# Kernel tuning notes

Hardware: AMD Instinct MI355X
Metric: run time of the kernel (lower is better)

Reference implementation:

```python
import jax, jax.numpy as jnp
import numpy as np

NUM_CLASSES = 100
CACHE_SIZE = 50
N_PROTOS = NUM_CLASSES * CACHE_SIZE  # 5000
FEAT_DIM = 128
BATCH = 2048
NVIEWS = 2
TEMP = 0.1
EPSILON = 0.05
PROTO_M = 0.99
TOPK = 10
LAMBDA_PCON = 1.0
SINKHORN_ITERS = 3


def _l1norm(x, axis):
    return x / jnp.clip(jnp.sum(jnp.abs(x), axis=axis, keepdims=True), 1e-12)


def _l2norm(x, axis=-1):
    return x / jnp.clip(jnp.linalg.norm(x, axis=axis, keepdims=True), 1e-12)


def _sinkhorn(feats, protos):
    # torch uses out.detach(): Q carries no gradient
    out = jax.lax.stop_gradient(feats @ protos.T)  # [N, K]
    Q = jnp.exp(out / EPSILON).T                   # [K, N]
    K_, B_ = Q.shape
    Q = Q / jnp.sum(Q)
    for _ in range(SINKHORN_ITERS):
        Q = _l1norm(Q, axis=1) / K_   # row L1 normalize
        Q = _l1norm(Q, axis=0) / B_   # col L1 normalize
    return (Q * B_).T                 # [N, K]


def _topk_mask(x, k):
    _, idx = jax.lax.top_k(x, k)
    rows = jnp.arange(x.shape[0])[:, None]
    return jnp.zeros_like(x).at[rows, idx].set(1.0)


def reference(features, targets, beta, protos):
    # features: [B, V, D] -> [V*B, D] (view-major, matches torch.cat(torch.unbind(dim=1)))
    feats = jnp.transpose(features, (1, 0, 2)).reshape(-1, FEAT_DIM)
    labels = jnp.tile(targets, NVIEWS)                              # [N]
    contrast_labels = jnp.tile(jnp.arange(NUM_CLASSES), CACHE_SIZE)  # [K]
    mask = (labels[:, None] == contrast_labels[None, :]).astype(feats.dtype)  # [N, K]

    # ---- mle_loss ----
    Q = _sinkhorn(feats, jax.lax.stop_gradient(protos))
    update_mask = mask * Q
    tkm = _topk_mask(update_mask, TOPK)
    update_mask = _l1norm(tkm * update_mask, axis=1)

    update_features = update_mask.T @ feats                         # [K, D]
    protos_new = PROTO_M * protos + (1.0 - PROTO_M) * update_features
    sim_mean = jax.lax.stop_gradient(
        jnp.mean(jnp.sum(_l2norm(update_features, 1) * _l2norm(protos, 1), axis=1)))
    protos2 = _l2norm(protos_new, axis=1)

    Q2 = _sinkhorn(feats, jax.lax.stop_gradient(protos2))
    logits = jax.nn.softplus(feats @ jax.lax.stop_gradient(protos2).T / TEMP)  # [N, K]

    loss_mask = mask * Q2
    # NOTE: original code top-ks update_mask (already normalized) here, not loss_mask
    tkm2 = _topk_mask(update_mask, TOPK)
    loss_mask = _l1norm(tkm2 * loss_mask, axis=1)
    masked_logits = loss_mask * logits

    positive_logits = mask * logits
    negative_logits = logits * (1.0 - mask)
    imp = jax.lax.stop_gradient(jnp.exp(beta * jnp.log(negative_logits + 1e-10)))
    total_logits = positive_logits + imp * negative_logits

    pos = jnp.sum(masked_logits, axis=1)                             # [N]
    neg = jnp.log(jnp.sum(jnp.exp(total_logits), axis=1, keepdims=True))  # [N, 1]
    # faithful to the torch broadcast: [N] - [N,1] -> [N, N]
    mle = -jnp.mean(pos - neg)

    # ---- proto_contra ----
    pn = _l2norm(protos2, axis=1)                                    # [K, D]
    plabels = jnp.tile(jnp.arange(NUM_CLASSES), CACHE_SIZE)
    pmask = (plabels[:, None] == plabels[None, :]).astype(pn.dtype)
    tau = jax.lax.stop_gradient((1.0 + (0.5 - sim_mean)) * 0.4)
    adc = pn @ pn.T / tau
    lg = adc - jax.lax.stop_gradient(jnp.max(adc, axis=1, keepdims=True))
    lmask = 1.0 - jnp.eye(N_PROTOS, dtype=pn.dtype)
    pmask = pmask * lmask
    ppos = jnp.sum(_l1norm(pmask, axis=1) * lg, axis=1)
    pneg = jnp.log(jnp.sum(lmask * jnp.exp(lg), axis=1))
    pcon = -jnp.mean(ppos - pneg)

    return mle + LAMBDA_PCON * pcon


def setup_inputs() -> dict:
    key = jax.random.key(0)
    k1, k2, k3 = jax.random.split(key, 3)
    features = jax.random.normal(k1, (BATCH, NVIEWS, FEAT_DIM), dtype=jnp.float32)
    features = _l2norm(features, axis=-1)  # unit-norm embeddings keep exp(./eps) finite
    targets = jax.random.randint(k2, (BATCH,), 0, NUM_CLASSES)
    beta = jnp.float32(0.5)
    protos = _l2norm(jax.random.uniform(k3, (N_PROTOS, FEAT_DIM), dtype=jnp.float32), axis=-1)
    return {"features": features, "targets": targets, "beta": beta, "protos": protos}
```

## Files before the change

kernel.cpp:

```cpp
#include <hip/hip_runtime.h>
#include <math.h>

constexpr int NUM_CLASSES = 100;
constexpr int CACHE_SIZE  = 50;
constexpr int NPROT       = 5000;
constexpr int FD          = 128;
constexpr int BATCH       = 2048;
constexpr int NROWS       = 4096;
constexpr int TOPK        = 10;
constexpr float INV_EPS   = 20.0f;
constexpr float INV_TEMP  = 10.0f;
constexpr float PROTO_M   = 0.99f;
constexpr int PLD         = 5120;
constexpr int SROWS       = 16;
constexpr int NSLOT       = NROWS / SROWS;
constexpr int NTILE       = 40;
constexpr int NTRI        = NTILE * (NTILE + 1) / 2;

typedef __attribute__((ext_vector_type(8))) short bf16x8;
typedef __attribute__((ext_vector_type(4))) float f32x4;
typedef __attribute__((ext_vector_type(4))) _Float16 f16x4;
typedef __attribute__((ext_vector_type(8))) _Float16 f16x8;

__device__ __forceinline__ float blockReduceSum(float v) {
  __shared__ float tmp[8];
  const int lane = threadIdx.x & 63;
  const int wid  = threadIdx.x >> 6;
  #pragma unroll
  for (int o = 32; o > 0; o >>= 1) v += __shfl_down(v, o, 64);
  __syncthreads();
  if (lane == 0) tmp[wid] = v;
  __syncthreads();
  const int nw = (blockDim.x + 63) >> 6;
  float s = 0.f;
  for (int i = 0; i < nw; ++i) s += tmp[i];
  return s;
}

__device__ __forceinline__ short f2bf(float x) {
  union { float f; unsigned u; } v; v.f = x;
  const unsigned r = v.u + 0x7fffu + ((v.u >> 16) & 1u);
  return (short)(r >> 16);
}
__device__ __forceinline__ float bf2f(short h) {
  union { float f; unsigned u; } v; v.u = ((unsigned)(unsigned short)h) << 16;
  return v.f;
}

__device__ __forceinline__ float fast_softplus(float x) {
  return fmaxf(x, 0.f) + __logf(1.f + __expf(-fabsf(x)));
}

__global__ void k_build_split(const float* __restrict__ features,
                              const float* __restrict__ protos,
                              float* __restrict__ feats,
                              short* __restrict__ fhi, short* __restrict__ flo,
                              short* __restrict__ phi, short* __restrict__ plo) {
  constexpr int NF4 = NROWS * (FD / 4);
  constexpr int NP4 = NPROT * FD / 4;
  const int t = blockIdx.x * 256 + threadIdx.x;
  if (t < NF4) {
    const int n  = t >> 5;
    const int d4 = (t & 31) << 2;
    const int b  = n & (BATCH - 1);
    const int v  = n >> 11;
    const float4 src = *reinterpret_cast<const float4*>(features + ((size_t)b * 2 + v) * FD + d4);
    *reinterpret_cast<float4*>(feats + (size_t)n * FD + d4) = src;
    short4 h, l;
    h.x = f2bf(src.x); l.x = f2bf(src.x - bf2f(h.x));
    h.y = f2bf(src.y); l.y = f2bf(src.y - bf2f(h.y));
    h.z = f2bf(src.z); l.z = f2bf(src.z - bf2f(h.z));
    h.w = f2bf(src.w); l.w = f2bf(src.w - bf2f(h.w));
    *reinterpret_cast<short4*>(fhi + (size_t)n * FD + d4) = h;
    *reinterpret_cast<short4*>(flo + (size_t)n * FD + d4) = l;
  } else if (t - NF4 < NP4) {
    const int u = t - NF4;
    const float4 v = *reinterpret_cast<const float4*>(protos + (size_t)u * 4);
    short4 h, l;
    h.x = f2bf(v.x); l.x = f2bf(v.x - bf2f(h.x));
    h.y = f2bf(v.y); l.y = f2bf(v.y - bf2f(h.y));
    h.z = f2bf(v.z); l.z = f2bf(v.z - bf2f(h.z));
    h.w = f2bf(v.w); l.w = f2bf(v.w - bf2f(h.w));
    *reinterpret_cast<short4*>(phi + (size_t)u * 4) = h;
    *reinterpret_cast<short4*>(plo + (size_t)u * 4) = l;
  }
}

__global__ __launch_bounds__(256) void k_gemm_mfma(
    const short* __restrict__ Ahi, const short* __restrict__ Alo,
    const short* __restrict__ Bhi, const short* __restrict__ Blo,
    int Nb, _Float16* __restrict__ C, float* __restrict__ colpart) {
  __shared__ __align__(16) short Bs[2][128 * 64];
  __shared__ float red[4][128];
  const int tid  = threadIdx.x;
  const int wid  = tid >> 6;
  const int lane = tid & 63;
  const int lr   = lane & 15;
  const int kg   = lane >> 4;
  const int m0   = blockIdx.y * 128 + wid * 32;
  const int n0   = blockIdx.x * 128;

  f32x4 acc[2][8];
  #pragma unroll
  for (int i = 0; i < 2; ++i)
    #pragma unroll
    for (int j = 0; j < 8; ++j) acc[i][j] = (f32x4){0.f, 0.f, 0.f, 0.f};

  bool cval[8];
  #pragma unroll
  for (int j = 0; j < 8; ++j) cval[j] = (n0 + j * 16 + lr < Nb);

  const int scol = tid >> 1;
  const int sk   = (tid & 1) * 32;
  const int gcol = min(n0 + scol, Nb - 1);

  #pragma unroll
  for (int h = 0; h < 2; ++h) {
    const int k0 = h * 64;
    if (h) __syncthreads();
    #pragma unroll
    for (int u = 0; u < 4; ++u) {
      const int kk2 = sk + u * 8;
      const bf16x8 vh = *reinterpret_cast<const bf16x8*>(Bhi + (size_t)gcol * FD + k0 + kk2);
      const bf16x8 vl = *reinterpret_cast<const bf16x8*>(Blo + (size_t)gcol * FD + k0 + kk2);
      const int byteoff = (scol * 128 + kk2 * 2) ^ ((scol & 7) << 4);
      *reinterpret_cast<bf16x8*>(reinterpret_cast<char*>(&Bs[0][0]) + byteoff) = vh;
      *reinterpret_cast<bf16x8*>(reinterpret_cast<char*>(&Bs[1][0]) + byteoff) = vl;
    }
    __syncthreads();
    #pragma unroll
    for (int kk = 0; kk < 2; ++kk) {
      const int kb = k0 + kk * 32 + kg * 8;
      bf16x8 ah[2], al[2], bh[8], bl[8];
      #pragma unroll
      for (int i = 0; i < 2; ++i) {
        const size_t off = (size_t)(m0 + i * 16 + lr) * FD + kb;
        ah[i] = *reinterpret_cast<const bf16x8*>(Ahi + off);
        al[i] = *reinterpret_cast<const bf16x8*>(Alo + off);
      }
      #pragma unroll
      for (int j = 0; j < 8; ++j) {
        const int col = j * 16 + lr;
        const int bo = (col * 128 + (kk * 32 + kg * 8) * 2) ^ ((col & 7) << 4);
        bh[j] = *reinterpret_cast<const bf16x8*>(reinterpret_cast<const char*>(&Bs[0][0]) + bo);
        bl[j] = *reinterpret_cast<const bf16x8*>(reinterpret_cast<const char*>(&Bs[1][0]) + bo);
      }
      #pragma unroll
      for (int i = 0; i < 2; ++i)
        #pragma unroll
        for (int j = 0; j < 8; ++j) {
          acc[i][j] = __builtin_amdgcn_mfma_f32_16x16x32_bf16(ah[i], bh[j], acc[i][j], 0, 0, 0);
          acc[i][j] = __builtin_amdgcn_mfma_f32_16x16x32_bf16(ah[i], bl[j], acc[i][j], 0, 0, 0);
          acc[i][j] = __builtin_amdgcn_mfma_f32_16x16x32_bf16(al[i], bh[j], acc[i][j], 0, 0, 0);
        }
    }
  }

  float csum[8];
  #pragma unroll
  for (int j = 0; j < 8; ++j) csum[j] = 0.f;
  #pragma unroll
  for (int i = 0; i < 2; ++i) {
    const int rbase = m0 + i * 16 + kg * 4;
    #pragma unroll
    for (int j = 0; j < 8; ++j) {
      if (!cval[j]) continue;
      const int col = n0 + j * 16 + lr;
      #pragma unroll
      for (int q = 0; q < 4; ++q) {
        const _Float16 hv = (_Float16)acc[i][j][q];
        C[(size_t)(rbase + q) * NPROT + col] = hv;
        csum[j] += __expf((float)hv * INV_EPS);
      }
    }
  }
  __syncthreads();
  #pragma unroll
  for (int j = 0; j < 8; ++j) {
    float v = csum[j];
    v += __shfl_xor(v, 16, 64);
    v += __shfl_xor(v, 32, 64);
    if (lane < 16) red[wid][j * 16 + lane] = v;
  }
  __syncthreads();
  if (tid < 128) {
    const int col = n0 + tid;
    if (col < Nb) {
      const float t = red[0][tid] + red[1][tid] + red[2][tid] + red[3][tid];
      colpart[(size_t)blockIdx.y * PLD + col] = t;
    }
  }
}

template <bool WITH_MLE>
__global__ __launch_bounds__(512) void k_sink_fused(const _Float16* __restrict__ big,
                                                    const float* __restrict__ Rin,
                                                    float* __restrict__ part,
                                                    float* __restrict__ semain,
                                                    const float* __restrict__ beta_ptr) {
  __shared__ float Cl[SROWS];
  const int r0   = blockIdx.x * SROWS;
  const int wid  = threadIdx.x >> 6;
  const int lane = threadIdx.x & 63;
  float beta = 0.f;
  bool bhalf = false;
  if constexpr (WITH_MLE) {
    beta = beta_ptr[0];
    bhalf = (beta == 0.5f);
  }
  #pragma unroll
  for (int rr = 0; rr < SROWS / 8; ++rr) {
    const int r = rr * 8 + wid;
    const _Float16* row = big + (size_t)(r0 + r) * NPROT;
    float s = 0.f, se = 0.f;
    for (int idx = lane; idx < NPROT / 8; idx += 64) {
      const f16x8 v = *reinterpret_cast<const f16x8*>(row + idx * 8);
      const float4 q0 = *reinterpret_cast<const float4*>(Rin + idx * 8);
      const float4 q1 = *reinterpret_cast<const float4*>(Rin + idx * 8 + 4);
      float ro[8];
      #pragma unroll
      for (int e = 0; e < 8; ++e) ro[e] = (float)v[e];
      s = fmaf(__expf(ro[0] * INV_EPS), q0.x, s);
      s = fmaf(__expf(ro[1] * INV_EPS), q0.y, s);
      s = fmaf(__expf(ro[2] * INV_EPS), q0.z, s);
      s = fmaf(__expf(ro[3] * INV_EPS), q0.w, s);
      s = fmaf(__expf(ro[4] * INV_EPS), q1.x, s);
      s = fmaf(__expf(ro[5] * INV_EPS), q1.y, s);
      s = fmaf(__expf(ro[6] * INV_EPS), q1.z, s);
      s = fmaf(__expf(ro[7] * INV_EPS), q1.w, s);
      if constexpr (WITH_MLE) {
        #pragma unroll
        for (int e = 0; e < 8; ++e) {
          const float x = ro[e] * INV_TEMP;
          const float l = fast_softplus(x);
          const float lb = l + 1e-10f;
          const float imp = bhalf ? sqrtf(lb) : __expf(beta * __logf(lb));
          se += __expf(imp * l);
        }
      }
    }
    #pragma unroll
    for (int o = 32; o > 0; o >>= 1) {
      s += __shfl_down(s, o, 64);
      if constexpr (WITH_MLE) se += __shfl_down(se, o, 64);
    }
    if (lane == 0) {
      Cl[r] = 1.0f / s;
      if constexpr (WITH_MLE) semain[r0 + r] = se;
    }
  }
  __syncthreads();
  for (int k4 = threadIdx.x * 4; k4 < NPROT; k4 += 2048) {
    float s[4] = {0.f, 0.f, 0.f, 0.f};
    #pragma unroll
    for (int r = 0; r < SROWS; ++r) {
      const f16x4 v = *reinterpret_cast<const f16x4*>(big + (size_t)(r0 + r) * NPROT + k4);
      const float c = Cl[r];
      #pragma unroll
      for (int e = 0; e < 4; ++e) s[e] = fmaf(__expf((float)v[e] * INV_EPS), c, s[e]);
    }
    *reinterpret_cast<float4*>(part + (size_t)blockIdx.x * PLD + k4) =
        make_float4(s[0], s[1], s[2], s[3]);
  }
}

__global__ __launch_bounds__(512) void k_red_slots(const float* __restrict__ part,
                                                   int nslots, float* __restrict__ R) {
  __shared__ float red[8][64];
  const int g  = threadIdx.x >> 6;
  const int kk = threadIdx.x & 63;
  const int k  = blockIdx.x * 64 + kk;
  float s = 0.f;
  if (k < NPROT) {
    const int per = nslots >> 3;
    const int b0 = g * per, b1 = b0 + per;
    for (int b = b0; b < b1; ++b) s += part[(size_t)b * PLD + k];
  }
  red[g][kk] = s;
  __syncthreads();
  if (threadIdx.x < 64 && k < NPROT) {
    float t = 0.f;
    #pragma unroll
    for (int g2 = 0; g2 < 8; ++g2) t += red[g2][kk];
    R[k] = 1.0f / t;
  }
}

__global__ __launch_bounds__(256) void k_top10(const _Float16* __restrict__ out1,
                                               const float* __restrict__ R3,
                                               const int* __restrict__ targets,
                                               float* __restrict__ wsel) {
  const int n = blockIdx.x * 4 + (threadIdx.x >> 6);
  const int lane = threadIdx.x & 63;
  const int c = targets[n & (BATCH - 1)];
  float cur = -1.0f, orig = -1.0f;
  if (lane < CACHE_SIZE) {
    const int k = c + lane * NUM_CLASSES;
    cur = __expf((float)out1[(size_t)n * NPROT + k] * INV_EPS) * R3[k];
    orig = cur;
  }
  float tvsum = 0.f;
  bool selme = false;
  #pragma unroll
  for (int i = 0; i < TOPK; ++i) {
    float bv = cur;
    int   bj = lane;
    #pragma unroll
    for (int o = 32; o > 0; o >>= 1) {
      const float ov = __shfl_xor(bv, o, 64);
      const int   oj = __shfl_xor(bj, o, 64);
      if (ov > bv || (ov == bv && oj < bj)) { bv = ov; bj = oj; }
    }
    tvsum += bv;
    if (lane == bj) { cur = -2.0f; selme = true; }
  }
  tvsum = fmaxf(tvsum, 1e-12f);
  if (lane < CACHE_SIZE)
    wsel[(size_t)n * CACHE_SIZE + lane] = selme ? orig / tvsum : 0.f;
}

__global__ __launch_bounds__(1024) void k_prep(const int* __restrict__ targets,
                                               int* __restrict__ classbase,
                                               int* __restrict__ rowlist) {
  __shared__ int t[BATCH];
  __shared__ short chcnt[8][NUM_CLASSES];
  __shared__ int   chpre[8][NUM_CLASSES];
  __shared__ int   ctot[NUM_CLASSES];
  __shared__ int   base[NUM_CLASSES + 1];
  for (int i = threadIdx.x; i < BATCH; i += 1024) t[i] = targets[i];
  __syncthreads();
  if (threadIdx.x < 8 * NUM_CLASSES) {
    const int ch = threadIdx.x / NUM_CLASSES;
    const int c  = threadIdx.x % NUM_CLASSES;
    int m = 0;
    const int i0 = ch << 8;
    for (int i = i0; i < i0 + 256; ++i) m += (t[i] == c);
    chcnt[ch][c] = (short)m;
  }
  __syncthreads();
  if (threadIdx.x < NUM_CLASSES) {
    const int c = threadIdx.x;
    int s = 0;
    #pragma unroll
    for (int ch = 0; ch < 8; ++ch) { chpre[ch][c] = s; s += chcnt[ch][c]; }
    ctot[c] = s;
  }
  __syncthreads();
  if (threadIdx.x == 0) {
    int s = 0;
    for (int c = 0; c < NUM_CLASSES; ++c) { base[c] = s; s += 2 * ctot[c]; }
    base[NUM_CLASSES] = s;
  }
  __syncthreads();
  if (threadIdx.x <= NUM_CLASSES) classbase[threadIdx.x] = base[threadIdx.x];
  for (int b = threadIdx.x; b < BATCH; b += 1024) {
    const int c  = t[b];
    const int ch = b >> 8;
    int r = chpre[ch][c];
    for (int i = ch << 8; i < b; ++i) r += (t[i] == c);
    const int bs  = base[c];
    const int cnt = (base[c + 1] - bs) >> 1;
    rowlist[bs + r] = b;
    rowlist[bs + cnt + r] = BATCH + b;
  }
}

__global__ __launch_bounds__(128) void k_ufpu(const float* __restrict__ feats,
                                              const float* __restrict__ wsel,
                                              const int* __restrict__ rowlist,
                                              const int* __restrict__ classbase,
                                              const float* __restrict__ protos,
                                              short* __restrict__ pnhi,
                                              short* __restrict__ pnlo,
                                              float* __restrict__ simbuf) {
  const int k = blockIdx.x;
  const int d = threadIdx.x;
  const int c = k % NUM_CLASSES;
  const int j = k / NUM_CLASSES;
  const int b0 = classbase[c], b1 = classbase[c + 1];
  float u = 0.f;
  for (int ii = b0; ii < b1; ++ii) {
    const int n = rowlist[ii];
    const float wv = wsel[(size_t)n * CACHE_SIZE + j];
    if (wv != 0.f) u = fmaf(wv, feats[(size_t)n * FD + d], u);
  }
  const float p = protos[(size_t)k * FD + d];
  const float pnew = PROTO_M * p + (1.0f - PROTO_M) * u;
  const float spp = blockReduceSum(p * p);
  const float suu = blockReduceSum(u * u);
  const float sup = blockReduceSum(u * p);
  const float snn = blockReduceSum(pnew * pnew);
  const float x = pnew / fmaxf(sqrtf(snn), 1e-12f);
  const short h = f2bf(x);
  pnhi[(size_t)k * FD + d] = h;
  pnlo[(size_t)k * FD + d] = f2bf(x - bf2f(h));
  if (d == 0)
    simbuf[k] = sup / (fmaxf(sqrtf(suu), 1e-12f) * fmaxf(sqrtf(spp), 1e-12f));
}

__global__ void k_tau(const float* __restrict__ simbuf, float* __restrict__ scalars) {
  float s = 0.f;
  for (int k = threadIdx.x; k < NPROT; k += 256) s += simbuf[k];
  s = blockReduceSum(s);
  if (threadIdx.x == 0) {
    const float sim_mean = s / (float)NPROT;
    scalars[0] = (1.0f + (0.5f - sim_mean)) * 0.4f;
  }
}

__global__ __launch_bounds__(256) void k_mle_fin(const _Float16* __restrict__ out2,
                                                 const float* __restrict__ R3,
                                                 const int* __restrict__ targets,
                                                 const float* __restrict__ wsel,
                                                 const float* __restrict__ beta_ptr,
                                                 const float* __restrict__ semain,
                                                 float* __restrict__ rowres) {
  const int n = blockIdx.x * 4 + (threadIdx.x >> 6);
  const int lane = threadIdx.x & 63;
  const int c = targets[n & (BATCH - 1)];
  const float beta = beta_ptr[0];
  const bool bhalf = (beta == 0.5f);
  float corr = 0.f, swl = 0.f, sw = 0.f;
  if (lane < CACHE_SIZE) {
    const int k = c + lane * NUM_CLASSES;
    const float o = (float)out2[(size_t)n * NPROT + k];
    const float x = o * INV_TEMP;
    const float l = fast_softplus(x);
    const float lb = l + 1e-10f;
    const float imp = bhalf ? sqrtf(lb) : __expf(beta * __logf(lb));
    corr = __expf(l) - __expf(imp * l);
    if (wsel[(size_t)n * CACHE_SIZE + lane] > 0.f) {
      const float w2 = __expf(o * INV_EPS) * R3[k];
      swl = w2 * l;
      sw  = w2;
    }
  }
  #pragma unroll
  for (int o = 32; o > 0; o >>= 1) {
    corr += __shfl_down(corr, o, 64);
    swl  += __shfl_down(swl,  o, 64);
    sw   += __shfl_down(sw,   o, 64);
  }
  if (lane == 0)
    rowres[n] = __logf(semain[n] + corr) - swl / fmaxf(sw, 1e-12f);
}

__global__ __launch_bounds__(256) void k_pcon_mfma(
    const short* __restrict__ Phi, const short* __restrict__ Plo,
    const float* __restrict__ scalars,
    float* __restrict__ part_neg, float* __restrict__ part_pos) {
  __shared__ __align__(16) short Bs[2][128 * 64];
  int tdec = blockIdx.x, by = 0;
  while (tdec >= NTILE - by) { tdec -= NTILE - by; ++by; }
  const int bx = by + tdec;
  const bool diag = (bx == by);

  const int tid  = threadIdx.x;
  const int wid  = tid >> 6;
  const int lane = tid & 63;
  const int lr   = lane & 15;
  const int kg   = lane >> 4;
  const int k0r  = by * 128 + wid * 32;
  const int l0   = bx * 128;
  const float invtau = 1.0f / scalars[0];

  f32x4 acc[2][8];
  #pragma unroll
  for (int i = 0; i < 2; ++i)
    #pragma unroll
    for (int j = 0; j < 8; ++j) acc[i][j] = (f32x4){0.f, 0.f, 0.f, 0.f};

  int rowa[2];
  #pragma unroll
  for (int i = 0; i < 2; ++i) {
    const int r = k0r + i * 16 + lr;
    rowa[i] = (r < NPROT) ? r : (NPROT - 1);
  }
  bool cval[8];
  #pragma unroll
  for (int j = 0; j < 8; ++j) cval[j] = (l0 + j * 16 + lr < NPROT);

  const int scol = tid >> 1;
  const int sk   = (tid & 1) * 32;
  const int gcol = min(l0 + scol, NPROT - 1);

  #pragma unroll
  for (int h = 0; h < 2; ++h) {
    const int k0 = h * 64;
    if (h) __syncthreads();
    #pragma unroll
    for (int u = 0; u < 4; ++u) {
      const int kk2 = sk + u * 8;
      const bf16x8 vh = *reinterpret_cast<const bf16x8*>(Phi + (size_t)gcol * FD + k0 + kk2);
      const bf16x8 vl = *reinterpret_cast<const bf16x8*>(Plo + (size_t)gcol * FD + k0 + kk2);
      const int byteoff = (scol * 128 + kk2 * 2) ^ ((scol & 7) << 4);
      *reinterpret_cast<bf16x8*>(reinterpret_cast<char*>(&Bs[0][0]) + byteoff) = vh;
      *reinterpret_cast<bf16x8*>(reinterpret_cast<char*>(&Bs[1][0]) + byteoff) = vl;
    }
    __syncthreads();
    #pragma unroll
    for (int kk = 0; kk < 2; ++kk) {
      const int kb = k0 + kk * 32 + kg * 8;
      bf16x8 ah[2], al[2], bh[8], bl[8];
      #pragma unroll
      for (int i = 0; i < 2; ++i) {
        const size_t off = (size_t)rowa[i] * FD + kb;
        ah[i] = *reinterpret_cast<const bf16x8*>(Phi + off);
        al[i] = *reinterpret_cast<const bf16x8*>(Plo + off);
      }
      #pragma unroll
      for (int j = 0; j < 8; ++j) {
        const int col = j * 16 + lr;
        const int bo = (col * 128 + (kk * 32 + kg * 8) * 2) ^ ((col & 7) << 4);
        bh[j] = *reinterpret_cast<const bf16x8*>(reinterpret_cast<const char*>(&Bs[0][0]) + bo);
        bl[j] = *reinterpret_cast<const bf16x8*>(reinterpret_cast<const char*>(&Bs[1][0]) + bo);
      }
      #pragma unroll
      for (int i = 0; i < 2; ++i)
        #pragma unroll
        for (int j = 0; j < 8; ++j) {
          acc[i][j] = __builtin_amdgcn_mfma_f32_16x16x32_bf16(ah[i], bh[j], acc[i][j], 0, 0, 0);
          acc[i][j] = __builtin_amdgcn_mfma_f32_16x16x32_bf16(ah[i], bl[j], acc[i][j], 0, 0, 0);
          acc[i][j] = __builtin_amdgcn_mfma_f32_16x16x32_bf16(al[i], bh[j], acc[i][j], 0, 0, 0);
        }
    }
  }

  int ccls[8];
  #pragma unroll
  for (int j = 0; j < 8; ++j) ccls[j] = (l0 + j * 16 + lr) % NUM_CLASSES;
  float cneg[8], cpos[8];
  #pragma unroll
  for (int j = 0; j < 8; ++j) { cneg[j] = 0.f; cpos[j] = 0.f; }

  #pragma unroll
  for (int i = 0; i < 2; ++i) {
    float sneg[4] = {0.f, 0.f, 0.f, 0.f};
    float spos[4] = {0.f, 0.f, 0.f, 0.f};
    const int rbase = k0r + i * 16 + kg * 4;
    #pragma unroll
    for (int q = 0; q < 4; ++q) {
      const int rg = rbase + q;
      if (rg >= NPROT) continue;
      const int rcls = rg % NUM_CLASSES;
      #pragma unroll
      for (int j = 0; j < 8; ++j) {
        const int cg = l0 + j * 16 + lr;
        if (!cval[j]) continue;
        if (diag && cg == rg) continue;
        const float lg = fmaf(acc[i][j][q], invtau, -invtau);
        const float e  = __expf(lg);
        sneg[q] += e;
        cneg[j] += e;
        if (ccls[j] == rcls) { spos[q] += lg; cpos[j] += lg; }
      }
    }
    #pragma unroll
    for (int q = 0; q < 4; ++q) {
      float sn = sneg[q], sp = spos[q];
      #pragma unroll
      for (int off = 8; off > 0; off >>= 1) {
        sn += __shfl_xor(sn, off, 64);
        sp += __shfl_xor(sp, off, 64);
      }
      if (lr == 0) {
        const int rg = rbase + q;
        if (rg < NPROT) {
          part_neg[(size_t)bx * PLD + rg] = sn;
          part_pos[(size_t)bx * PLD + rg] = sp;
        }
      }
    }
  }

  if (!diag) {
    __syncthreads();
    float* redn = reinterpret_cast<float*>(&Bs[0][0]);
    float* redp = redn + 512;
    #pragma unroll
    for (int j = 0; j < 8; ++j) {
      float cn = cneg[j];
      cn += __shfl_xor(cn, 16, 64);
      cn += __shfl_xor(cn, 32, 64);
      float cp = cpos[j];
      cp += __shfl_xor(cp, 16, 64);
      cp += __shfl_xor(cp, 32, 64);
      if (lane < 16) {
        redn[wid * 128 + j * 16 + lane] = cn;
        redp[wid * 128 + j * 16 + lane] = cp;
      }
    }
    __syncthreads();
    if (tid < 128) {
      const int cg = l0 + tid;
      if (cg < NPROT) {
        const float tn = redn[tid] + redn[128 + tid] + redn[256 + tid] + redn[384 + tid];
        const float tp = redp[tid] + redp[128 + tid] + redp[256 + tid] + redp[384 + tid];
        part_neg[(size_t)by * PLD + cg] = tn;
        part_pos[(size_t)by * PLD + cg] = tp;
      }
    }
  }
}

__global__ __launch_bounds__(256) void k_pcon_fin(const float* __restrict__ part_neg,
                                                  const float* __restrict__ part_pos,
                                                  float* __restrict__ pconbuf) {
  __shared__ float rn[4][64], rp[4][64];
  const int g  = threadIdx.x >> 6;
  const int kk = threadIdx.x & 63;
  const int k  = blockIdx.x * 64 + kk;
  float sn = 0.f, sp = 0.f;
  if (k < NPROT) {
    for (int b = g * 10; b < g * 10 + 10; ++b) {
      sn += part_neg[(size_t)b * PLD + k];
      sp += part_pos[(size_t)b * PLD + k];
    }
  }
  rn[g][kk] = sn; rp[g][kk] = sp;
  __syncthreads();
  if (threadIdx.x < 64 && k < NPROT) {
    const float tn = rn[0][kk] + rn[1][kk] + rn[2][kk] + rn[3][kk];
    const float tp = rp[0][kk] + rp[1][kk] + rp[2][kk] + rp[3][kk];
    pconbuf[k] = __logf(tn) - tp * (1.0f / (float)(CACHE_SIZE - 1));
  }
}

__global__ void k_final(const float* __restrict__ rowres,
                        const float* __restrict__ pconbuf,
                        float* __restrict__ outp) {
  float s1 = 0.f, s2 = 0.f;
  for (int i = threadIdx.x; i < NROWS; i += 256) s1 += rowres[i];
  for (int i = threadIdx.x; i < NPROT; i += 256) s2 += pconbuf[i];
  s1 = blockReduceSum(s1);
  s2 = blockReduceSum(s2);
  if (threadIdx.x == 0) outp[0] = s1 / (float)NROWS + s2 / (float)NPROT;
}

extern "C" void kernel_launch(void* const* d_in, const int* in_sizes, int n_in,
                              void* d_out, int out_size, void* d_ws, size_t ws_size,
                              hipStream_t stream) {
  (void)in_sizes; (void)n_in; (void)out_size; (void)ws_size;
  const float* features = (const float*)d_in[0];
  const int*   targets  = (const int*)d_in[1];
  const float* beta     = (const float*)d_in[2];
  const float* protos   = (const float*)d_in[3];
  float* outp = (float*)d_out;

  char* basep = (char*)d_ws;
  size_t off = 0;
  auto alloc = [&](size_t bytes) -> void* {
    void* p = basep + off;
    off = (off + bytes + 255) & ~(size_t)255;
    return p;
  };
  _Float16* big  = (_Float16*)alloc((size_t)NROWS * NPROT * 2);
  float* feats   = (float*)alloc((size_t)NROWS * FD * 4);
  short* fhi     = (short*)alloc((size_t)NROWS * FD * 2);
  short* flo     = (short*)alloc((size_t)NROWS * FD * 2);
  short* phi     = (short*)alloc((size_t)NPROT * FD * 2);
  short* plo     = (short*)alloc((size_t)NPROT * FD * 2);
  float* part    = (float*)alloc((size_t)NSLOT * PLD * 4);
  float* Rk      = (float*)alloc(NPROT * 4);
  float* wsel    = (float*)alloc((size_t)NROWS * CACHE_SIZE * 4);
  int*   rowlist = (int*)alloc(NROWS * 4);
  int*   classbase = (int*)alloc((NUM_CLASSES + 1) * 4);
  float* simbuf  = (float*)alloc(NPROT * 4);
  float* scalars = (float*)alloc(64);
  float* semain  = (float*)alloc(NROWS * 4);
  float* rowres  = (float*)alloc(NROWS * 4);
  float* pconbuf = (float*)alloc(NPROT * 4);
  float* pneg    = (float*)alloc((size_t)NTILE * PLD * 4);
  float* ppos    = (float*)alloc((size_t)NTILE * PLD * 4);

  k_build_split<<<1138, 256, 0, stream>>>(features, protos, feats, fhi, flo, phi, plo);
  k_prep<<<1, 1024, 0, stream>>>(targets, classbase, rowlist);

  k_gemm_mfma<<<dim3(40, 32), 256, 0, stream>>>(fhi, flo, phi, plo, NPROT, big, part);
  k_red_slots<<<79, 512, 0, stream>>>(part, 32, Rk);
  k_sink_fused<false><<<NSLOT, 512, 0, stream>>>(big, Rk, part, nullptr, nullptr);
  k_red_slots<<<79, 512, 0, stream>>>(part, NSLOT, Rk);
  k_sink_fused<false><<<NSLOT, 512, 0, stream>>>(big, Rk, part, nullptr, nullptr);
  k_red_slots<<<79, 512, 0, stream>>>(part, NSLOT, Rk);

  k_top10<<<NROWS / 4, 256, 0, stream>>>(big, Rk, targets, wsel);
  k_ufpu<<<NPROT, 128, 0, stream>>>(feats, wsel, rowlist, classbase, protos, phi, plo, simbuf);
  k_tau<<<1, 256, 0, stream>>>(simbuf, scalars);

  k_gemm_mfma<<<dim3(40, 32), 256, 0, stream>>>(fhi, flo, phi, plo, NPROT, big, part);
  k_red_slots<<<79, 512, 0, stream>>>(part, 32, Rk);
  k_sink_fused<false><<<NSLOT, 512, 0, stream>>>(big, Rk, part, nullptr, nullptr);
  k_red_slots<<<79, 512, 0, stream>>>(part, NSLOT, Rk);
  k_sink_fused<true><<<NSLOT, 512, 0, stream>>>(big, Rk, part, semain, beta);
  k_red_slots<<<79, 512, 0, stream>>>(part, NSLOT, Rk);

  k_mle_fin<<<NROWS / 4, 256, 0, stream>>>(big, Rk, targets, wsel, beta, semain, rowres);
  k_pcon_mfma<<<NTRI, 256, 0, stream>>>(phi, plo, scalars, pneg, ppos);
  k_pcon_fin<<<79, 256, 0, stream>>>(pneg, ppos, pconbuf);
  k_final<<<1, 256, 0, stream>>>(rowres, pconbuf, outp);
}
```

Baseline: 316.3 us.

## Share one exp between Sinkhorn and softplus terms; halve rows per sinkhorn block

Because INV_EPS is twice INV_TEMP, exp(o*INV_EPS) is computed as t*t where t = exp(o*INV_TEMP). Softplus becomes log(1+t) and exp(softplus) becomes 1+t, which removes several transcendental calls per element in the fused sinkhorn kernel and in the final MLE kernel. SROWS also drops from 16 to 8, so each block handles one row per wave and twice as many blocks launch. Skipping the stable softplus form risks overflow or precision loss when o*10 is large, though o stays within [-1,1] for unit-norm inputs.

```diff
diff --git a/kernel.cpp b/kernel.cpp
--- a/kernel.cpp
+++ b/kernel.cpp
@@ -12,7 +12,7 @@
 constexpr float INV_TEMP  = 10.0f;
 constexpr float PROTO_M   = 0.99f;
 constexpr int PLD         = 5120;
-constexpr int SROWS       = 16;
+constexpr int SROWS       = 8;
 constexpr int NSLOT       = NROWS / SROWS;
 constexpr int NTILE       = 40;
 constexpr int NTRI        = NTILE * (NTILE + 1) / 2;
@@ -208,35 +208,33 @@
     beta = beta_ptr[0];
     bhalf = (beta == 0.5f);
   }
-  #pragma unroll
-  for (int rr = 0; rr < SROWS / 8; ++rr) {
-    const int r = rr * 8 + wid;
+  {
+    const int r = wid;
     const _Float16* row = big + (size_t)(r0 + r) * NPROT;
     float s = 0.f, se = 0.f;
     for (int idx = lane; idx < NPROT / 8; idx += 64) {
       const f16x8 v = *reinterpret_cast<const f16x8*>(row + idx * 8);
       const float4 q0 = *reinterpret_cast<const float4*>(Rin + idx * 8);
       const float4 q1 = *reinterpret_cast<const float4*>(Rin + idx * 8 + 4);
-      float ro[8];
+      float ro[8], rq[8];
       #pragma unroll
       for (int e = 0; e < 8; ++e) ro[e] = (float)v[e];
-      s = fmaf(__expf(ro[0] * INV_EPS), q0.x, s);
-      s = fmaf(__expf(ro[1] * INV_EPS), q0.y, s);
-      s = fmaf(__expf(ro[2] * INV_EPS), q0.z, s);
-      s = fmaf(__expf(ro[3] * INV_EPS), q0.w, s);
-      s = fmaf(__expf(ro[4] * INV_EPS), q1.x, s);
-      s = fmaf(__expf(ro[5] * INV_EPS), q1.y, s);
-      s = fmaf(__expf(ro[6] * INV_EPS), q1.z, s);
-      s = fmaf(__expf(ro[7] * INV_EPS), q1.w, s);
+      rq[0] = q0.x; rq[1] = q0.y; rq[2] = q0.z; rq[3] = q0.w;
+      rq[4] = q1.x; rq[5] = q1.y; rq[6] = q1.z; rq[7] = q1.w;
       if constexpr (WITH_MLE) {
         #pragma unroll
         for (int e = 0; e < 8; ++e) {
-          const float x = ro[e] * INV_TEMP;
-          const float l = fast_softplus(x);
+          const float t = __expf(ro[e] * INV_TEMP);
+          s = fmaf(t * t, rq[e], s);
+          const float l = __logf(1.f + t);
           const float lb = l + 1e-10f;
           const float imp = bhalf ? sqrtf(lb) : __expf(beta * __logf(lb));
           se += __expf(imp * l);
         }
+      } else {
+        #pragma unroll
+        for (int e = 0; e < 8; ++e)
+          s = fmaf(__expf(ro[e] * INV_EPS), rq[e], s);
       }
     }
     #pragma unroll
@@ -424,13 +422,13 @@
   if (lane < CACHE_SIZE) {
     const int k = c + lane * NUM_CLASSES;
     const float o = (float)out2[(size_t)n * NPROT + k];
-    const float x = o * INV_TEMP;
-    const float l = fast_softplus(x);
+    const float t = __expf(o * INV_TEMP);
+    const float l = __logf(1.f + t);
     const float lb = l + 1e-10f;
     const float imp = bhalf ? sqrtf(lb) : __expf(beta * __logf(lb));
-    corr = __expf(l) - __expf(imp * l);
+    corr = (1.f + t) - __expf(imp * l);
     if (wsel[(size_t)n * CACHE_SIZE + lane] > 0.f) {
-      const float w2 = __expf(o * INV_EPS) * R3[k];
+      const float w2 = t * t * R3[k];
       swl = w2 * l;
       sw  = w2;
     }
```

After: 333.0 us. 1.05x slower.
